# Kernel optimization log

Hardware: AMD Instinct MI355X
Metric: run time of the kernel (lower is better)

Reference implementation:

```python
import jax, jax.numpy as jnp
import numpy as np
from jax import lax

B, T, D_IN, H = 32, 2048, 256, 512

def setup_inputs() -> dict:
    key = jax.random.key(0)
    k = jax.random.split(key, 6)
    s = 1.0 / np.sqrt(H)
    return {
        "X":   jax.random.normal(k[0], (B, T, D_IN), dtype=jnp.float32),
        "Wxh": jax.random.normal(k[1], (D_IN, H), dtype=jnp.float32) * s,
        "Whh": jax.random.normal(k[2], (H, H),   dtype=jnp.float32) * s,
        "bh":  jnp.zeros((H,), dtype=jnp.float32),
        "QW":  jax.random.uniform(k[3], (H, D_IN), dtype=jnp.float32),
        "KW":  jax.random.uniform(k[4], (H, D_IN), dtype=jnp.float32),
    }

def reference(X, Wxh, Whh, bh, QW, KW):
    # --- core: tanh Elman RNN, return_sequences=True ---
    Bsz = X.shape[0]
    Hdim = Whh.shape[0]
    xW = jnp.einsum('btd,dh->tbh', X, Wxh)          # precompute input projections, [T,B,H]
    def step(h, xw):
        h = jnp.tanh(xw + h @ Whh + bh)
        return h, h
    h0 = jnp.zeros((Bsz, Hdim), dtype=X.dtype)
    _, Y = lax.scan(step, h0, xW)                   # Y: [T,B,H] == stacked Yt list
    # --- forward_attention (batched form of the python-loop version) ---
    Q0 = Y[-1] @ QW                                 # [B, D_in]
    K = jnp.einsum('tbh,hd->tbd', Y, KW)            # [T, B, D_in]
    scores = jnp.tanh(jnp.einsum('bd,tbd->bt', Q0, K))  # AF = tanh (default)
    A = jax.nn.softmax(scores, axis=-1)             # softmax over timesteps
    c = jnp.einsum('bt,tbh->bh', A, Y)              # context vector
    # no FC (fc_layers=None): forward_uni returns (Yt, c)
    return Y, c
```

## Files before the change

### kernel.cpp

```cpp
#include <hip/hip_runtime.h>

#define BB 32
#define TT 2048
#define DD 256
#define HH 512
#define NSL 8
#define SLW 64
#define KPT 64

__device__ __forceinline__ float tanh_f(float x) {
    float e = __expf(2.f * x);
    return 1.f - 2.f / (e + 1.f);
}

__global__ __launch_bounds__(256) void xw_gemm(const float* __restrict__ X,
                                               const float* __restrict__ Wxh,
                                               const float* __restrict__ bh,
                                               float* __restrict__ out) {
    __shared__ float As[16][68];
    __shared__ float Bs[16][68];
    const int tid = threadIdx.x;
    const int r0 = blockIdx.x * 64;
    const int n0 = blockIdx.y * 64;
    const int ty = tid >> 4, tx = tid & 15;

    float acc[4][4];
#pragma unroll
    for (int i = 0; i < 4; i++)
#pragma unroll
        for (int j = 0; j < 4; j++) acc[i][j] = 0.f;

    const int arow = tid >> 2;
    const int akq  = (tid & 3) * 4;
    const int brow = tid >> 4;
    const int bq   = (tid & 15) * 4;

    for (int k0 = 0; k0 < DD; k0 += 16) {
        float4 a4 = *reinterpret_cast<const float4*>(
            &X[(size_t)(r0 + arow) * DD + k0 + akq]);
        As[akq + 0][arow] = a4.x;
        As[akq + 1][arow] = a4.y;
        As[akq + 2][arow] = a4.z;
        As[akq + 3][arow] = a4.w;
        float4 b4 = *reinterpret_cast<const float4*>(
            &Wxh[(size_t)(k0 + brow) * HH + n0 + bq]);
        *reinterpret_cast<float4*>(&Bs[brow][bq]) = b4;
        __syncthreads();
#pragma unroll
        for (int kk = 0; kk < 16; kk++) {
            float a0 = As[kk][ty * 4 + 0];
            float a1 = As[kk][ty * 4 + 1];
            float a2 = As[kk][ty * 4 + 2];
            float a3 = As[kk][ty * 4 + 3];
            float4 bv = *reinterpret_cast<const float4*>(&Bs[kk][tx * 4]);
            acc[0][0] += a0 * bv.x; acc[0][1] += a0 * bv.y; acc[0][2] += a0 * bv.z; acc[0][3] += a0 * bv.w;
            acc[1][0] += a1 * bv.x; acc[1][1] += a1 * bv.y; acc[1][2] += a1 * bv.z; acc[1][3] += a1 * bv.w;
            acc[2][0] += a2 * bv.x; acc[2][1] += a2 * bv.y; acc[2][2] += a2 * bv.z; acc[2][3] += a2 * bv.w;
            acc[3][0] += a3 * bv.x; acc[3][1] += a3 * bv.y; acc[3][2] += a3 * bv.z; acc[3][3] += a3 * bv.w;
        }
        __syncthreads();
    }
    float4 bias = *reinterpret_cast<const float4*>(&bh[n0 + tx * 4]);
#pragma unroll
    for (int i = 0; i < 4; i++) {
        int r = r0 + ty * 4 + i;
        int b = r >> 11;
        int t = r & (TT - 1);
        float4 o;
        o.x = acc[i][0] + bias.x;
        o.y = acc[i][1] + bias.y;
        o.z = acc[i][2] + bias.z;
        o.w = acc[i][3] + bias.w;
        *reinterpret_cast<float4*>(
            &out[((size_t)t * BB + b) * HH + n0 + tx * 4]) = o;
    }
}

__global__ __launch_bounds__(512) void scan_kernel(const float* __restrict__ Whh,
                                                   float* __restrict__ Y,
                                                   unsigned long long* __restrict__ ex) {
    __shared__ float h_lds[HH];
    __shared__ float part[NSL][SLW];
    const int tid = threadIdx.x;
    const int bid = blockIdx.x;
    const int s = bid >> 5;
    const int b = bid & 31;
    const int n0 = s * SLW;
    const int n  = tid & 63;
    const int kq = tid >> 6;
    const int k0 = kq * KPT;

    float w[KPT];
#pragma unroll
    for (int j = 0; j < KPT; j++)
        w[j] = Whh[(size_t)(k0 + j) * HH + n0 + n];

    h_lds[tid] = 0.f;
    __syncthreads();

    float xw_cur = 0.f;
    if (tid < SLW) xw_cur = Y[(size_t)b * HH + n0 + tid];

    const bool foreign = (kq != s);

    for (int t = 0; t < TT; t++) {
        float a0 = 0.f, a1 = 0.f, a2 = 0.f, a3 = 0.f;
#pragma unroll
        for (int j = 0; j < KPT; j += 4) {
            float4 h4 = *reinterpret_cast<const float4*>(&h_lds[k0 + j]);
            a0 += h4.x * w[j + 0];
            a1 += h4.y * w[j + 1];
            a2 += h4.z * w[j + 2];
            a3 += h4.w * w[j + 3];
        }
        part[kq][n] = (a0 + a1) + (a2 + a3);
        __syncthreads();

        if (tid < SLW) {
            float ssum = part[0][tid] + part[1][tid] + part[2][tid] + part[3][tid] +
                         part[4][tid] + part[5][tid] + part[6][tid] + part[7][tid] +
                         xw_cur;
            float hn = tanh_f(ssum);
            h_lds[n0 + tid] = hn;
            Y[((size_t)t * BB + b) * HH + n0 + tid] = hn;
            unsigned long long pk =
                ((unsigned long long)(unsigned)(t + 1) << 32) |
                (unsigned long long)__float_as_uint(hn);
            __hip_atomic_store(&ex[(((size_t)(t & 1) * BB + b) << 9) + n0 + tid],
                               pk, __ATOMIC_RELAXED, __HIP_MEMORY_SCOPE_AGENT);
        }

        if (t + 1 < TT) {
            if (tid < SLW)
                xw_cur = Y[((size_t)(t + 1) * BB + b) * HH + n0 + tid];
            if (foreign) {
                unsigned long long* p =
                    &ex[(((size_t)(t & 1) * BB + b) << 9) + tid];
                const unsigned want = (unsigned)(t + 1);
                unsigned long long v;
                do {
                    v = __hip_atomic_load(p, __ATOMIC_RELAXED,
                                          __HIP_MEMORY_SCOPE_AGENT);
                } while ((unsigned)(v >> 32) != want);
                h_lds[tid] = __uint_as_float((unsigned)v);
            }
            __syncthreads();
        }
    }
}

__global__ __launch_bounds__(512) void attn_kernel(const float* __restrict__ QW,
                                                   const float* __restrict__ KW,
                                                   const float* __restrict__ Y,
                                                   float* __restrict__ c) {
    __shared__ float yl[HH];
    __shared__ float q0[DD];
    __shared__ float vv[HH];
    __shared__ float sc[TT];
    __shared__ float red[16];
    const int tid = threadIdx.x;
    const int b = blockIdx.x;
    const int w = tid >> 6;
    const int l = tid & 63;

    if (tid < HH) yl[tid] = Y[((size_t)(TT - 1) * BB + b) * HH + tid];
    __syncthreads();

    if (tid < DD) {
        float s = 0.f;
#pragma unroll 8
        for (int h = 0; h < HH; h++) s += yl[h] * QW[(size_t)h * DD + tid];
        q0[tid] = s;
    }
    __syncthreads();

    {
        float s = 0.f;
        const int nn = tid;
#pragma unroll 4
        for (int d = 0; d < DD; d += 4) {
            float4 kw = *reinterpret_cast<const float4*>(&KW[(size_t)nn * DD + d]);
            float4 q4 = *reinterpret_cast<const float4*>(&q0[d]);
            s += kw.x * q4.x + kw.y * q4.y + kw.z * q4.z + kw.w * q4.w;
        }
        vv[nn] = s;
    }
    __syncthreads();

    for (int i = 0; i < TT / 8; i++) {
        int t = i * 8 + w;
        const float* yr = &Y[((size_t)t * BB + b) * HH + l * 8];
        float4 y0 = *reinterpret_cast<const float4*>(yr);
        float4 y1 = *reinterpret_cast<const float4*>(yr + 4);
        float4 v0 = *reinterpret_cast<const float4*>(&vv[l * 8]);
        float4 v1 = *reinterpret_cast<const float4*>(&vv[l * 8 + 4]);
        float s = y0.x * v0.x + y0.y * v0.y + y0.z * v0.z + y0.w * v0.w +
                  y1.x * v1.x + y1.y * v1.y + y1.z * v1.z + y1.w * v1.w;
#pragma unroll
        for (int off = 32; off > 0; off >>= 1) s += __shfl_xor(s, off);
        if (l == 0) sc[t] = tanh_f(s);
    }
    __syncthreads();

    float m = -1e30f;
    for (int i = tid; i < TT; i += 512) m = fmaxf(m, sc[i]);
#pragma unroll
    for (int off = 32; off > 0; off >>= 1) m = fmaxf(m, __shfl_xor(m, off));
    if (l == 0) red[w] = m;
    __syncthreads();
    float gm = red[0];
#pragma unroll
    for (int i = 1; i < 8; i++) gm = fmaxf(gm, red[i]);

    float ls = 0.f;
    for (int i = tid; i < TT; i += 512) {
        float e = __expf(sc[i] - gm);
        sc[i] = e;
        ls += e;
    }
#pragma unroll
    for (int off = 32; off > 0; off >>= 1) ls += __shfl_xor(ls, off);
    __syncthreads();
    if (l == 0) red[8 + w] = ls;
    __syncthreads();
    float tot = 0.f;
#pragma unroll
    for (int i = 0; i < 8; i++) tot += red[8 + i];
    float inv = 1.f / tot;
    for (int i = tid; i < TT; i += 512) sc[i] *= inv;
    __syncthreads();

    {
        const int nn = tid;
        float acc = 0.f;
        for (int t = 0; t < TT; t += 4) {
            float4 a4 = *reinterpret_cast<const float4*>(&sc[t]);
            acc += a4.x * Y[((size_t)(t + 0) * BB + b) * HH + nn];
            acc += a4.y * Y[((size_t)(t + 1) * BB + b) * HH + nn];
            acc += a4.z * Y[((size_t)(t + 2) * BB + b) * HH + nn];
            acc += a4.w * Y[((size_t)(t + 3) * BB + b) * HH + nn];
        }
        c[(size_t)b * HH + nn] = acc;
    }
}

extern "C" void kernel_launch(void* const* d_in, const int* in_sizes, int n_in,
                              void* d_out, int out_size, void* d_ws, size_t ws_size,
                              hipStream_t stream) {
    const float* X   = (const float*)d_in[0];
    const float* Wxh = (const float*)d_in[1];
    const float* Whh = (const float*)d_in[2];
    const float* bh  = (const float*)d_in[3];
    const float* QW  = (const float*)d_in[4];
    const float* KW  = (const float*)d_in[5];
    float* out  = (float*)d_out;
    float* Ybuf = out;
    float* cbuf = out + (size_t)TT * BB * HH;
    unsigned long long* ex = (unsigned long long*)d_ws;

    dim3 ga(BB * TT / 64, HH / 64);
    xw_gemm<<<ga, 256, 0, stream>>>(X, Wxh, bh, Ybuf);
    scan_kernel<<<BB * NSL, 512, 0, stream>>>(Whh, Ybuf, ex);
    attn_kernel<<<BB, 512, 0, stream>>>(QW, KW, Ybuf, cbuf);
}
```

Before: 3.362 ms.

## Poll exchange buffer via L2 with MALL fallback and drop per-step barrier

The cross-block hidden-state exchange now stores each value twice, once with an sc0 L2-scoped store and once with an agent-scope atomic store. All threads, including those of the block's own slice, poll with an sc0 L2 load and switch permanently to agent-scope atomic loads after a spin limit. The second __syncthreads per step is replaced by double-buffered partial sums and an lgkmcnt wait, aiming to cut synchronization latency on the serial recurrence. The risk is correctness: on MI355X, blocks on different XCDs have separate L2s, so L2-only polling relies on the fallback. Removing the barrier also leaves h_lds writes racing with other waves' reads of the next step.

```diff
diff --git a/kernel.cpp b/kernel.cpp
--- a/kernel.cpp
+++ b/kernel.cpp
@@ -11,6 +11,23 @@
 __device__ __forceinline__ float tanh_f(float x) {
     float e = __expf(2.f * x);
     return 1.f - 2.f / (e + 1.f);
+}
+
+__device__ __forceinline__ unsigned long long poll_l2(const unsigned long long* p) {
+    unsigned long long v;
+    asm volatile("global_load_dwordx2 %0, %1, off sc0\n\t"
+                 "s_waitcnt vmcnt(0)"
+                 : "=v"(v) : "v"(p) : "memory");
+    return v;
+}
+__device__ __forceinline__ void store_l2(unsigned long long* p, unsigned long long v) {
+    asm volatile("global_store_dwordx2 %0, %1, off sc0" :: "v"(p), "v"(v) : "memory");
+}
+__device__ __forceinline__ unsigned long long mall_load(const unsigned long long* p) {
+    return __hip_atomic_load(p, __ATOMIC_RELAXED, __HIP_MEMORY_SCOPE_AGENT);
+}
+__device__ __forceinline__ void mall_store(unsigned long long* p, unsigned long long v) {
+    __hip_atomic_store(p, v, __ATOMIC_RELAXED, __HIP_MEMORY_SCOPE_AGENT);
 }
 
 __global__ __launch_bounds__(256) void xw_gemm(const float* __restrict__ X,
@@ -80,30 +97,32 @@
                                                    float* __restrict__ Y,
                                                    unsigned long long* __restrict__ ex) {
     __shared__ float h_lds[HH];
-    __shared__ float part[NSL][SLW];
+    __shared__ float part[2][NSL][SLW];
     const int tid = threadIdx.x;
     const int bid = blockIdx.x;
     const int s = bid >> 5;
     const int b = bid & 31;
     const int n0 = s * SLW;
-    const int n  = tid & 63;
+    const int lane = tid & 63;
     const int kq = tid >> 6;
     const int k0 = kq * KPT;
 
     float w[KPT];
 #pragma unroll
     for (int j = 0; j < KPT; j++)
-        w[j] = Whh[(size_t)(k0 + j) * HH + n0 + n];
+        w[j] = Whh[(size_t)(k0 + j) * HH + n0 + lane];
 
     h_lds[tid] = 0.f;
     __syncthreads();
 
+    const bool red = (kq == 0);
     float xw_cur = 0.f;
-    if (tid < SLW) xw_cur = Y[(size_t)b * HH + n0 + tid];
-
-    const bool foreign = (kq != s);
+    if (red) xw_cur = Y[(size_t)b * HH + n0 + lane];
+
+    bool use_mall = false;
 
     for (int t = 0; t < TT; t++) {
+        const int p = t & 1;
         float a0 = 0.f, a1 = 0.f, a2 = 0.f, a3 = 0.f;
 #pragma unroll
         for (int j = 0; j < KPT; j += 4) {
@@ -113,38 +132,45 @@
             a2 += h4.z * w[j + 2];
             a3 += h4.w * w[j + 3];
         }
-        part[kq][n] = (a0 + a1) + (a2 + a3);
+        part[p][kq][lane] = (a0 + a1) + (a2 + a3);
         __syncthreads();
 
-        if (tid < SLW) {
-            float ssum = part[0][tid] + part[1][tid] + part[2][tid] + part[3][tid] +
-                         part[4][tid] + part[5][tid] + part[6][tid] + part[7][tid] +
-                         xw_cur;
+        if (red) {
+            float ssum = part[p][0][lane] + part[p][1][lane] +
+                         part[p][2][lane] + part[p][3][lane] +
+                         part[p][4][lane] + part[p][5][lane] +
+                         part[p][6][lane] + part[p][7][lane] + xw_cur;
             float hn = tanh_f(ssum);
-            h_lds[n0 + tid] = hn;
-            Y[((size_t)t * BB + b) * HH + n0 + tid] = hn;
             unsigned long long pk =
                 ((unsigned long long)(unsigned)(t + 1) << 32) |
                 (unsigned long long)__float_as_uint(hn);
-            __hip_atomic_store(&ex[(((size_t)(t & 1) * BB + b) << 9) + n0 + tid],
-                               pk, __ATOMIC_RELAXED, __HIP_MEMORY_SCOPE_AGENT);
+            unsigned long long* q = &ex[(((size_t)p * BB + b) << 9) + n0 + lane];
+            store_l2(q, pk);
+            mall_store(q, pk);
+            Y[((size_t)t * BB + b) * HH + n0 + lane] = hn;
+            if (t + 1 < TT)
+                xw_cur = Y[((size_t)(t + 1) * BB + b) * HH + n0 + lane];
         }
 
         if (t + 1 < TT) {
-            if (tid < SLW)
-                xw_cur = Y[((size_t)(t + 1) * BB + b) * HH + n0 + tid];
-            if (foreign) {
-                unsigned long long* p =
-                    &ex[(((size_t)(t & 1) * BB + b) << 9) + tid];
-                const unsigned want = (unsigned)(t + 1);
-                unsigned long long v;
+            unsigned long long* q = &ex[(((size_t)p * BB + b) << 9) + tid];
+            const unsigned want = (unsigned)(t + 1);
+            unsigned long long v = 0;
+            if (!use_mall) {
+                int spins = 0;
+                for (;;) {
+                    v = poll_l2(q);
+                    if ((unsigned)(v >> 32) == want) break;
+                    if (++spins > 1500) { use_mall = true; break; }
+                }
+            }
+            if (use_mall) {
                 do {
-                    v = __hip_atomic_load(p, __ATOMIC_RELAXED,
-                                          __HIP_MEMORY_SCOPE_AGENT);
+                    v = mall_load(q);
                 } while ((unsigned)(v >> 32) != want);
-                h_lds[tid] = __uint_as_float((unsigned)v);
             }
-            __syncthreads();
+            h_lds[tid] = __uint_as_float((unsigned)v);
+            asm volatile("s_waitcnt lgkmcnt(0)" ::: "memory");
         }
     }
 }
```

After: 4.102 ms. +22.0%, slower.

## Reduce scan partials via lane shuffles with double-buffered h and split attention kernels

Applied to the files above, without the earlier changes.

The scan kernel now gives each output column a group of 8 adjacent lanes, one per K-slice. Partial sums are combined with xor shuffles instead of an LDS partial array plus a barrier, and h is double-buffered in LDS so each step needs one barrier instead of two. The attention stage, previously 32 blocks doing serial work over 2048 timesteps, is split into five kernels (v projection, scores, softmax, chunked context, final reduce) to spread the Y reads across 256 blocks. The costs are extra kernel launches and workspace round trips, and the scan now has more spinning lanes (each polls one element across an 8-lane group).

```diff
diff --git a/kernel.cpp b/kernel.cpp
--- a/kernel.cpp
+++ b/kernel.cpp
@@ -6,11 +6,18 @@
 #define HH 512
 #define NSL 8
 #define SLW 64
-#define KPT 64
+#define CHW 68
 
 __device__ __forceinline__ float tanh_f(float x) {
     float e = __expf(2.f * x);
     return 1.f - 2.f / (e + 1.f);
+}
+
+__device__ __forceinline__ unsigned long long mall_load(const unsigned long long* p) {
+    return __hip_atomic_load(p, __ATOMIC_RELAXED, __HIP_MEMORY_SCOPE_AGENT);
+}
+__device__ __forceinline__ void mall_store(unsigned long long* p, unsigned long long v) {
+    __hip_atomic_store(p, v, __ATOMIC_RELAXED, __HIP_MEMORY_SCOPE_AGENT);
 }
 
 __global__ __launch_bounds__(256) void xw_gemm(const float* __restrict__ X,
@@ -79,91 +86,84 @@
 __global__ __launch_bounds__(512) void scan_kernel(const float* __restrict__ Whh,
                                                    float* __restrict__ Y,
                                                    unsigned long long* __restrict__ ex) {
-    __shared__ float h_lds[HH];
-    __shared__ float part[NSL][SLW];
+    __shared__ float h_lds[2][NSL][CHW];
     const int tid = threadIdx.x;
     const int bid = blockIdx.x;
     const int s = bid >> 5;
     const int b = bid & 31;
     const int n0 = s * SLW;
-    const int n  = tid & 63;
-    const int kq = tid >> 6;
-    const int k0 = kq * KPT;
-
-    float w[KPT];
-#pragma unroll
-    for (int j = 0; j < KPT; j++)
-        w[j] = Whh[(size_t)(k0 + j) * HH + n0 + n];
-
-    h_lds[tid] = 0.f;
-    __syncthreads();
-
-    float xw_cur = 0.f;
-    if (tid < SLW) xw_cur = Y[(size_t)b * HH + n0 + tid];
-
-    const bool foreign = (kq != s);
+    const int o  = tid >> 3;
+    const int ks = tid & 7;
+    const int k0 = ks * 64;
+    const bool fin = (ks == 0);
+    const bool foreign = (ks != s);
+
+    float w[64];
+#pragma unroll
+    for (int j = 0; j < 64; j++)
+        w[j] = Whh[(size_t)(k0 + j) * HH + n0 + o];
+
+    for (int i = tid; i < NSL * CHW; i += 512)
+        (&h_lds[0][0][0])[i] = 0.f;
+    __syncthreads();
+
+    float xw_cur = fin ? Y[(size_t)b * HH + n0 + o] : 0.f;
 
     for (int t = 0; t < TT; t++) {
+        const int p = t & 1;
+        const float* hp = h_lds[p][ks];
         float a0 = 0.f, a1 = 0.f, a2 = 0.f, a3 = 0.f;
 #pragma unroll
-        for (int j = 0; j < KPT; j += 4) {
-            float4 h4 = *reinterpret_cast<const float4*>(&h_lds[k0 + j]);
+        for (int j = 0; j < 64; j += 4) {
+            float4 h4 = *reinterpret_cast<const float4*>(&hp[j]);
             a0 += h4.x * w[j + 0];
             a1 += h4.y * w[j + 1];
             a2 += h4.z * w[j + 2];
             a3 += h4.w * w[j + 3];
         }
-        part[kq][n] = (a0 + a1) + (a2 + a3);
-        __syncthreads();
-
-        if (tid < SLW) {
-            float ssum = part[0][tid] + part[1][tid] + part[2][tid] + part[3][tid] +
-                         part[4][tid] + part[5][tid] + part[6][tid] + part[7][tid] +
-                         xw_cur;
-            float hn = tanh_f(ssum);
-            h_lds[n0 + tid] = hn;
-            Y[((size_t)t * BB + b) * HH + n0 + tid] = hn;
+        float sum = (a0 + a1) + (a2 + a3);
+        sum += __shfl_xor(sum, 1);
+        sum += __shfl_xor(sum, 2);
+        sum += __shfl_xor(sum, 4);
+
+        if (fin) {
+            float hn = tanh_f(sum + xw_cur);
             unsigned long long pk =
                 ((unsigned long long)(unsigned)(t + 1) << 32) |
                 (unsigned long long)__float_as_uint(hn);
-            __hip_atomic_store(&ex[(((size_t)(t & 1) * BB + b) << 9) + n0 + tid],
-                               pk, __ATOMIC_RELAXED, __HIP_MEMORY_SCOPE_AGENT);
+            mall_store(&ex[(((size_t)p * BB + b) << 9) + n0 + o], pk);
+            Y[((size_t)t * BB + b) * HH + n0 + o] = hn;
+            h_lds[p ^ 1][s][o] = hn;
+            if (t + 1 < TT)
+                xw_cur = Y[((size_t)(t + 1) * BB + b) * HH + n0 + o];
         }
 
         if (t + 1 < TT) {
-            if (tid < SLW)
-                xw_cur = Y[((size_t)(t + 1) * BB + b) * HH + n0 + tid];
             if (foreign) {
-                unsigned long long* p =
-                    &ex[(((size_t)(t & 1) * BB + b) << 9) + tid];
+                unsigned long long* q =
+                    &ex[(((size_t)p * BB + b) << 9) + k0 + o];
                 const unsigned want = (unsigned)(t + 1);
                 unsigned long long v;
                 do {
-                    v = __hip_atomic_load(p, __ATOMIC_RELAXED,
-                                          __HIP_MEMORY_SCOPE_AGENT);
+                    v = mall_load(q);
                 } while ((unsigned)(v >> 32) != want);
-                h_lds[tid] = __uint_as_float((unsigned)v);
+                h_lds[p ^ 1][ks][o] = __uint_as_float((unsigned)v);
             }
             __syncthreads();
         }
     }
 }
 
-__global__ __launch_bounds__(512) void attn_kernel(const float* __restrict__ QW,
-                                                   const float* __restrict__ KW,
-                                                   const float* __restrict__ Y,
-                                                   float* __restrict__ c) {
+__global__ __launch_bounds__(512) void attn_v(const float* __restrict__ QW,
+                                              const float* __restrict__ KW,
+                                              const float* __restrict__ Y,
+                                              float* __restrict__ vbuf) {
     __shared__ float yl[HH];
     __shared__ float q0[DD];
-    __shared__ float vv[HH];
-    __shared__ float sc[TT];
-    __shared__ float red[16];
     const int tid = threadIdx.x;
     const int b = blockIdx.x;
-    const int w = tid >> 6;
-    const int l = tid & 63;
-
-    if (tid < HH) yl[tid] = Y[((size_t)(TT - 1) * BB + b) * HH + tid];
+
+    yl[tid] = Y[((size_t)(TT - 1) * BB + b) * HH + tid];
     __syncthreads();
 
     if (tid < DD) {
@@ -174,36 +174,57 @@
     }
     __syncthreads();
 
-    {
-        float s = 0.f;
-        const int nn = tid;
+    float s = 0.f;
 #pragma unroll 4
-        for (int d = 0; d < DD; d += 4) {
-            float4 kw = *reinterpret_cast<const float4*>(&KW[(size_t)nn * DD + d]);
-            float4 q4 = *reinterpret_cast<const float4*>(&q0[d]);
-            s += kw.x * q4.x + kw.y * q4.y + kw.z * q4.z + kw.w * q4.w;
-        }
-        vv[nn] = s;
-    }
-    __syncthreads();
-
-    for (int i = 0; i < TT / 8; i++) {
-        int t = i * 8 + w;
+    for (int d = 0; d < DD; d += 4) {
+        float4 kw = *reinterpret_cast<const float4*>(&KW[(size_t)tid * DD + d]);
+        float4 q4 = *reinterpret_cast<const float4*>(&q0[d]);
+        s += kw.x * q4.x + kw.y * q4.y + kw.z * q4.z + kw.w * q4.w;
+    }
+    vbuf[(size_t)b * HH + tid] = s;
+}
+
+__global__ __launch_bounds__(512) void attn_sc(const float* __restrict__ Y,
+                                               const float* __restrict__ vbuf,
+                                               float* __restrict__ sc) {
+    __shared__ float vv[HH];
+    const int tid = threadIdx.x;
+    const int b = blockIdx.x >> 3;
+    const int t0 = (blockIdx.x & 7) * 256;
+    const int w = tid >> 6;
+    const int l = tid & 63;
+
+    vv[tid] = vbuf[(size_t)b * HH + tid];
+    __syncthreads();
+
+    float4 v0 = *reinterpret_cast<const float4*>(&vv[l * 8]);
+    float4 v1 = *reinterpret_cast<const float4*>(&vv[l * 8 + 4]);
+    for (int i = 0; i < 32; i++) {
+        int t = t0 + i * 8 + w;
         const float* yr = &Y[((size_t)t * BB + b) * HH + l * 8];
         float4 y0 = *reinterpret_cast<const float4*>(yr);
         float4 y1 = *reinterpret_cast<const float4*>(yr + 4);
-        float4 v0 = *reinterpret_cast<const float4*>(&vv[l * 8]);
-        float4 v1 = *reinterpret_cast<const float4*>(&vv[l * 8 + 4]);
         float s = y0.x * v0.x + y0.y * v0.y + y0.z * v0.z + y0.w * v0.w +
                   y1.x * v1.x + y1.y * v1.y + y1.z * v1.z + y1.w * v1.w;
 #pragma unroll
         for (int off = 32; off > 0; off >>= 1) s += __shfl_xor(s, off);
-        if (l == 0) sc[t] = tanh_f(s);
-    }
+        if (l == 0) sc[(size_t)b * TT + t] = tanh_f(s);
+    }
+}
+
+__global__ __launch_bounds__(512) void attn_sm(float* __restrict__ sc) {
+    __shared__ float sl[TT];
+    __shared__ float red[16];
+    const int tid = threadIdx.x;
+    const int b = blockIdx.x;
+    const int w = tid >> 6;
+    const int l = tid & 63;
+
+    for (int i = tid; i < TT; i += 512) sl[i] = sc[(size_t)b * TT + i];
     __syncthreads();
 
     float m = -1e30f;
-    for (int i = tid; i < TT; i += 512) m = fmaxf(m, sc[i]);
+    for (int i = tid; i < TT; i += 512) m = fmaxf(m, sl[i]);
 #pragma unroll
     for (int off = 32; off > 0; off >>= 1) m = fmaxf(m, __shfl_xor(m, off));
     if (l == 0) red[w] = m;
@@ -214,8 +235,8 @@
 
     float ls = 0.f;
     for (int i = tid; i < TT; i += 512) {
-        float e = __expf(sc[i] - gm);
-        sc[i] = e;
+        float e = __expf(sl[i] - gm);
+        sl[i] = e;
         ls += e;
     }
 #pragma unroll
@@ -227,21 +248,41 @@
 #pragma unroll
     for (int i = 0; i < 8; i++) tot += red[8 + i];
     float inv = 1.f / tot;
-    for (int i = tid; i < TT; i += 512) sc[i] *= inv;
-    __syncthreads();
-
-    {
-        const int nn = tid;
-        float acc = 0.f;
-        for (int t = 0; t < TT; t += 4) {
-            float4 a4 = *reinterpret_cast<const float4*>(&sc[t]);
-            acc += a4.x * Y[((size_t)(t + 0) * BB + b) * HH + nn];
-            acc += a4.y * Y[((size_t)(t + 1) * BB + b) * HH + nn];
-            acc += a4.z * Y[((size_t)(t + 2) * BB + b) * HH + nn];
-            acc += a4.w * Y[((size_t)(t + 3) * BB + b) * HH + nn];
-        }
-        c[(size_t)b * HH + nn] = acc;
-    }
+    for (int i = tid; i < TT; i += 512) sc[(size_t)b * TT + i] = sl[i] * inv;
+}
+
+__global__ __launch_bounds__(512) void attn_ctx(const float* __restrict__ Y,
+                                                const float* __restrict__ sc,
+                                                float* __restrict__ cpart) {
+    __shared__ float al[256];
+    const int tid = threadIdx.x;
+    const int b = blockIdx.x >> 3;
+    const int ch = blockIdx.x & 7;
+    const int t0 = ch * 256;
+
+    if (tid < 256) al[tid] = sc[(size_t)b * TT + t0 + tid];
+    __syncthreads();
+
+    float acc = 0.f;
+    for (int i = 0; i < 256; i += 4) {
+        float4 a4 = *reinterpret_cast<const float4*>(&al[i]);
+        acc += a4.x * Y[((size_t)(t0 + i + 0) * BB + b) * HH + tid];
+        acc += a4.y * Y[((size_t)(t0 + i + 1) * BB + b) * HH + tid];
+        acc += a4.z * Y[((size_t)(t0 + i + 2) * BB + b) * HH + tid];
+        acc += a4.w * Y[((size_t)(t0 + i + 3) * BB + b) * HH + tid];
+    }
+    cpart[((size_t)blockIdx.x) * HH + tid] = acc;
+}
+
+__global__ __launch_bounds__(512) void attn_fin(const float* __restrict__ cpart,
+                                                float* __restrict__ c) {
+    const int tid = threadIdx.x;
+    const int b = blockIdx.x;
+    float acc = 0.f;
+#pragma unroll
+    for (int ch = 0; ch < 8; ch++)
+        acc += cpart[((size_t)(b * 8 + ch)) * HH + tid];
+    c[(size_t)b * HH + tid] = acc;
 }
 
 extern "C" void kernel_launch(void* const* d_in, const int* in_sizes, int n_in,
@@ -256,10 +297,19 @@
     float* out  = (float*)d_out;
     float* Ybuf = out;
     float* cbuf = out + (size_t)TT * BB * HH;
-    unsigned long long* ex = (unsigned long long*)d_ws;
+
+    char* ws = (char*)d_ws;
+    unsigned long long* ex = (unsigned long long*)ws;
+    float* vbuf  = (float*)(ws + (2 * BB * HH) * 8);
+    float* scbuf = (float*)(ws + 262144 + 65536);
+    float* cpart = (float*)(ws + 262144 + 65536 + 262144);
 
     dim3 ga(BB * TT / 64, HH / 64);
     xw_gemm<<<ga, 256, 0, stream>>>(X, Wxh, bh, Ybuf);
     scan_kernel<<<BB * NSL, 512, 0, stream>>>(Whh, Ybuf, ex);
-    attn_kernel<<<BB, 512, 0, stream>>>(QW, KW, Ybuf, cbuf);
-}
+    attn_v<<<BB, 512, 0, stream>>>(QW, KW, Ybuf, vbuf);
+    attn_sc<<<BB * 8, 512, 0, stream>>>(Ybuf, vbuf, scbuf);
+    attn_sm<<<BB, 512, 0, stream>>>(scbuf);
+    attn_ctx<<<BB * 8, 512, 0, stream>>>(Ybuf, scbuf, cpart);
+    attn_fin<<<BB, 512, 0, stream>>>(cpart, cbuf);
+}
```

New measurement: 4.240 ms. +26.1%, slower.
